# Performance work log

Measured on AMD Instinct MI355X. Metric: run time of the kernel, lower is better.

The kernel has to match this reference:

```python
import jax, jax.numpy as jnp
import numpy as np

HEADS = 8
D_MODEL = 512
D_K = D_MODEL // HEADS


def setup_inputs() -> dict:
    key = jax.random.key(0)
    ks = jax.random.split(key, 12)
    B, S = 2, 4096
    scale = 1.0 / np.sqrt(D_MODEL)
    inp = {
        "q": jax.random.normal(ks[0], (B, S, D_MODEL), jnp.float32),
        "k": jax.random.normal(ks[1], (B, S, D_MODEL), jnp.float32),
        "v": jax.random.normal(ks[2], (B, S, D_MODEL), jnp.float32),
        "mask": jax.random.randint(ks[3], (B, 1, 1, S), 0, 2, jnp.int32),
        "wq": jax.random.normal(ks[4], (D_MODEL, D_MODEL), jnp.float32) * scale,
        "bq": jnp.zeros((D_MODEL,), jnp.float32),
        "wk": jax.random.normal(ks[5], (D_MODEL, D_MODEL), jnp.float32) * scale,
        "bk": jnp.zeros((D_MODEL,), jnp.float32),
        "wv": jax.random.normal(ks[6], (D_MODEL, D_MODEL), jnp.float32) * scale,
        "bv": jnp.zeros((D_MODEL,), jnp.float32),
        "wo": jax.random.normal(ks[7], (D_MODEL, D_MODEL), jnp.float32) * scale,
        "bo": jnp.zeros((D_MODEL,), jnp.float32),
    }
    return inp


def reference(q, k, v, mask, wq, bq, wk, bk, wv, bv, wo, bo):
    B, S, _ = q.shape
    # torch nn.Linear: y = x @ W.T + b
    qh = (q @ wq.T + bq).reshape(B, S, HEADS, D_K).transpose(0, 2, 1, 3)  # b h s d
    kh = (k @ wk.T + bk).reshape(B, S, HEADS, D_K).transpose(0, 2, 1, 3)
    vh = (v @ wv.T + bv).reshape(B, S, HEADS, D_K).transpose(0, 2, 1, 3)
    scores = jnp.einsum("bhqd,bhkd->bhqk", qh, kh) / jnp.sqrt(jnp.float32(D_K))
    scores = jnp.where(mask == 0, jnp.float32(-1e9), scores)
    attn = jax.nn.softmax(scores, axis=-1)  # dropout is identity in eval mode
    out = jnp.einsum("bhqk,bhkd->bhqd", attn, vh)
    out = out.transpose(0, 2, 1, 3).reshape(B, S, D_MODEL)
    return out @ wo.T + bo
```

## Files before the change

### kernel.cpp

```cpp
#include <hip/hip_runtime.h>
#include <hip/hip_bf16.h>

#define S 4096
#define DM 512
#define HH 8
#define DK 64
#define MT 8192

typedef __attribute__((ext_vector_type(8)))  short bf16x8;
typedef __attribute__((ext_vector_type(4)))  float f32x4;
typedef __attribute__((ext_vector_type(16))) float f32x16;
typedef __attribute__((ext_vector_type(4)))  unsigned int u32x4;

#define CQ 0.18033688011112042f

__device__ __forceinline__ short f2bs(float x) {
    __hip_bfloat16 h = __float2bfloat16(x);
    return *reinterpret_cast<short*>(&h);
}

__device__ __forceinline__ bf16x8 pack8(const float4& a, const float4& b) {
    bf16x8 r;
    r[0] = f2bs(a.x); r[1] = f2bs(a.y); r[2] = f2bs(a.z); r[3] = f2bs(a.w);
    r[4] = f2bs(b.x); r[5] = f2bs(b.y); r[6] = f2bs(b.z); r[7] = f2bs(b.w);
    return r;
}

__device__ __forceinline__ unsigned cvtpk(float lo, float hi) {
    unsigned r;
    asm("v_cvt_pk_bf16_f32 %0, %1, %2" : "=v"(r) : "v"(lo), "v"(hi));
    return r;
}

__device__ __forceinline__ bf16x8 mk_pb(unsigned a, unsigned b, unsigned c, unsigned d) {
    u32x4 t; t[0] = a; t[1] = b; t[2] = c; t[3] = d;
    return __builtin_bit_cast(bf16x8, t);
}

__global__ __launch_bounds__(256, 4)
void qkv_gemm(const float* __restrict__ Xq, const float* __restrict__ Xk,
              const float* __restrict__ Xv,
              const float* __restrict__ Wq, const float* __restrict__ Wk,
              const float* __restrict__ Wv,
              const float* __restrict__ Bq, const float* __restrict__ Bk,
              const float* __restrict__ Bv,
              const int* __restrict__ mask, float* __restrict__ maskf,
              unsigned short* __restrict__ Yq, unsigned short* __restrict__ Yk,
              unsigned short* __restrict__ Yv)
{
    __shared__ char As[128 * 128];
    __shared__ char Bs[64 * 128];
    const int bid  = blockIdx.x;
    const int t = threadIdx.x;
    if (bid < 32) {
        int i = bid * 256 + t;
        maskf[i] = mask[i] ? 0.f : -3e38f;
    }
    const int work = (bid & 7) * 192 + (bid >> 3);
    const int gp   = work >> 3;
    const int mat  = gp >> 6;
    const int m0   = (gp & 63) * 128;
    const int n0   = (work & 7) * 64;
    const float* X    = mat == 0 ? Xq : (mat == 1 ? Xk : Xv);
    const float* W    = mat == 0 ? Wq : (mat == 1 ? Wk : Wv);
    const float* bias = mat == 0 ? Bq : (mat == 1 ? Bk : Bv);

    const int l = t & 63, w = t >> 6;
    const int wr = w >> 1, wc = w & 1;
    const int lr = l & 15, lg = l >> 4;
    const int srow = t >> 3, schk = t & 7;
    const int sswz = (schk ^ (srow & 7)) * 16;

    float4 fA[4][2]; float4 fB[2][2];
    auto loadA = [&](int k0) {
        #pragma unroll
        for (int i = 0; i < 4; ++i) {
            const float* p = X + (size_t)(m0 + srow + 32 * i) * DM + k0 + schk * 8;
            fA[i][0] = *(const float4*)p;
            fA[i][1] = *(const float4*)(p + 4);
        }
    };
    auto loadB = [&](int k0) {
        #pragma unroll
        for (int i = 0; i < 2; ++i) {
            const float* p = W + (size_t)(n0 + srow + 32 * i) * DM + k0 + schk * 8;
            fB[i][0] = *(const float4*)p;
            fB[i][1] = *(const float4*)(p + 4);
        }
    };

    loadA(0); loadB(0);

    f32x4 acc[4][2];
    #pragma unroll
    for (int fm = 0; fm < 4; ++fm)
        #pragma unroll
        for (int fn = 0; fn < 2; ++fn) acc[fm][fn] = f32x4{0.f, 0.f, 0.f, 0.f};

    #pragma unroll
    for (int kt = 0; kt < 8; ++kt) {
        bf16x8 wA[4], wB[2];
        #pragma unroll
        for (int i = 0; i < 4; ++i) wA[i] = pack8(fA[i][0], fA[i][1]);
        #pragma unroll
        for (int i = 0; i < 2; ++i) wB[i] = pack8(fB[i][0], fB[i][1]);

        if (kt < 7) { loadA((kt + 1) * 64); loadB((kt + 1) * 64); }

        __syncthreads();
        #pragma unroll
        for (int i = 0; i < 4; ++i)
            *(bf16x8*)(As + (srow + 32 * i) * 128 + sswz) = wA[i];
        #pragma unroll
        for (int i = 0; i < 2; ++i)
            *(bf16x8*)(Bs + (srow + 32 * i) * 128 + sswz) = wB[i];
        __syncthreads();

        #pragma unroll
        for (int kc = 0; kc < 2; ++kc) {
            bf16x8 af[4], bfr[2];
            #pragma unroll
            for (int fm = 0; fm < 4; ++fm) {
                int row = wr * 64 + fm * 16 + lr;
                af[fm] = *(const bf16x8*)(As + row * 128 + (((kc * 4 + lg) ^ (row & 7)) * 16));
            }
            #pragma unroll
            for (int fn = 0; fn < 2; ++fn) {
                int row = wc * 32 + fn * 16 + lr;
                bfr[fn] = *(const bf16x8*)(Bs + row * 128 + (((kc * 4 + lg) ^ (row & 7)) * 16));
            }
            #pragma unroll
            for (int fm = 0; fm < 4; ++fm)
                #pragma unroll
                for (int fn = 0; fn < 2; ++fn)
                    acc[fm][fn] = __builtin_amdgcn_mfma_f32_16x16x32_bf16(af[fm], bfr[fn], acc[fm][fn], 0, 0, 0);
        }
    }

    #pragma unroll
    for (int fm = 0; fm < 4; ++fm) {
        #pragma unroll
        for (int fn = 0; fn < 2; ++fn) {
            int n = n0 + wc * 32 + fn * 16 + lr;
            float bn = bias[n];
            int mbase = m0 + wr * 64 + fm * 16 + lg * 4;
            int h = n >> 6, d = n & 63;
            int bb = mbase >> 12, s0 = mbase & (S - 1);
            if (mat == 0) {
                #pragma unroll
                for (int r = 0; r < 4; ++r)
                    Yq[(((size_t)(bb * HH + h)) * S + s0 + r) * DK + d] =
                        (unsigned short)f2bs((acc[fm][fn][r] + bn) * CQ);
            } else if (mat == 1) {
                int c   = (d >> 4) & 3;
                int hi2 = (d >> 3) & 1;
                int ii  = d & 7;
                size_t blkb = ((((size_t)(bb * HH + h)) * 128 + (s0 >> 5)) * 4 + c) * 512;
                int lanebase = (s0 & 31) + 32 * hi2;
                #pragma unroll
                for (int r = 0; r < 4; ++r)
                    Yk[blkb + (size_t)(lanebase + r) * 8 + ii] =
                        (unsigned short)f2bs(acc[fm][fn][r] + bn);
            } else {
                int dt2  = (d >> 5) & 1;
                int hi_s = (s0 >> 3) & 1;
                int lane = (d & 31) + 32 * hi_s;
                size_t base = ((((size_t)(bb * HH + h)) * 256 + (s0 >> 4)) * 2 + dt2) * 512
                            + (size_t)lane * 8 + (s0 & 7);
                ushort4 u;
                u.x = (unsigned short)f2bs(acc[fm][fn][0] + bn);
                u.y = (unsigned short)f2bs(acc[fm][fn][1] + bn);
                u.z = (unsigned short)f2bs(acc[fm][fn][2] + bn);
                u.w = (unsigned short)f2bs(acc[fm][fn][3] + bn);
                *(ushort4*)(Yv + base) = u;
            }
        }
    }
}

__global__ __launch_bounds__(256, 2)
void out_gemm(const short* __restrict__ Xb, const float* __restrict__ W,
              const float* __restrict__ bias, float* __restrict__ Y)
{
    __shared__ char As[128 * 128];
    __shared__ char Bs[64 * 128];
    const int bid  = blockIdx.x;
    const int work = (bid & 7) * 64 + (bid >> 3);
    const int n0 = (work & 7) * 64;
    const int m0 = (work >> 3) * 128;

    const int t = threadIdx.x, l = t & 63, w = t >> 6;
    const int wr = w >> 1, wc = w & 1;
    const int lr = l & 15, lg = l >> 4;
    const int srow = t >> 3, schk = t & 7;
    const int sswz = (schk ^ (srow & 7)) * 16;

    float4 fB[2][2]; bf16x8 rA[4];
    auto loadA = [&](int k0) {
        #pragma unroll
        for (int i = 0; i < 4; ++i)
            rA[i] = *(const bf16x8*)(Xb + (size_t)(m0 + srow + 32 * i) * DM + k0 + schk * 8);
    };
    auto loadB = [&](int k0) {
        #pragma unroll
        for (int i = 0; i < 2; ++i) {
            const float* p = W + (size_t)(n0 + srow + 32 * i) * DM + k0 + schk * 8;
            fB[i][0] = *(const float4*)p;
            fB[i][1] = *(const float4*)(p + 4);
        }
    };

    loadA(0); loadB(0);

    f32x4 acc[4][2];
    #pragma unroll
    for (int fm = 0; fm < 4; ++fm)
        #pragma unroll
        for (int fn = 0; fn < 2; ++fn) acc[fm][fn] = f32x4{0.f, 0.f, 0.f, 0.f};

    #pragma unroll
    for (int kt = 0; kt < 8; ++kt) {
        bf16x8 wA[4], wB[2];
        #pragma unroll
        for (int i = 0; i < 4; ++i) wA[i] = rA[i];
        #pragma unroll
        for (int i = 0; i < 2; ++i) wB[i] = pack8(fB[i][0], fB[i][1]);

        if (kt < 7) { loadA((kt + 1) * 64); loadB((kt + 1) * 64); }

        __syncthreads();
        #pragma unroll
        for (int i = 0; i < 4; ++i)
            *(bf16x8*)(As + (srow + 32 * i) * 128 + sswz) = wA[i];
        #pragma unroll
        for (int i = 0; i < 2; ++i)
            *(bf16x8*)(Bs + (srow + 32 * i) * 128 + sswz) = wB[i];
        __syncthreads();

        #pragma unroll
        for (int kc = 0; kc < 2; ++kc) {
            bf16x8 af[4], bfr[2];
            #pragma unroll
            for (int fm = 0; fm < 4; ++fm) {
                int row = wr * 64 + fm * 16 + lr;
                af[fm] = *(const bf16x8*)(As + row * 128 + (((kc * 4 + lg) ^ (row & 7)) * 16));
            }
            #pragma unroll
            for (int fn = 0; fn < 2; ++fn) {
                int row = wc * 32 + fn * 16 + lr;
                bfr[fn] = *(const bf16x8*)(Bs + row * 128 + (((kc * 4 + lg) ^ (row & 7)) * 16));
            }
            #pragma unroll
            for (int fm = 0; fm < 4; ++fm)
                #pragma unroll
                for (int fn = 0; fn < 2; ++fn)
                    acc[fm][fn] = __builtin_amdgcn_mfma_f32_16x16x32_bf16(af[fm], bfr[fn], acc[fm][fn], 0, 0, 0);
        }
    }

    #pragma unroll
    for (int fm = 0; fm < 4; ++fm) {
        #pragma unroll
        for (int fn = 0; fn < 2; ++fn) {
            int n = n0 + wc * 32 + fn * 16 + lr;
            float bn = bias[n];
            int mbase = m0 + wr * 64 + fm * 16 + lg * 4;
            #pragma unroll
            for (int r = 0; r < 4; ++r)
                Y[(size_t)(mbase + r) * DM + n] = acc[fm][fn][r] + bn;
        }
    }
}

__global__ __launch_bounds__(256, 4)
void flash_mfma(const short* __restrict__ qh,
                const short* __restrict__ kfb,
                const short* __restrict__ vfb,
                const float* __restrict__ maskf,
                unsigned short* __restrict__ att)
{
    const int bid  = blockIdx.x;
    const int work = (bid & 7) * 128 + (bid >> 3);
    const int bh = work >> 6, b = bh >> 3, h = bh & 7;
    const int q0 = (work & 63) * 64;
    const int t = threadIdx.x, w = t >> 6, l = t & 63;
    const int l31 = l & 31, hi = l >> 5;
    const int kw = w & 1, qw = w >> 1;

    __shared__ float scr[2 * 64 * 33];

    const short* qg = qh + ((size_t)bh * S + q0 + qw * 32 + l31) * DK;
    bf16x8 qf[4];
    #pragma unroll
    for (int c = 0; c < 4; ++c)
        qf[c] = *(const bf16x8*)(qg + c * 16 + hi * 8);

    f32x16 oc[2];
    #pragma unroll
    for (int dt = 0; dt < 2; ++dt)
        #pragma unroll
        for (int r = 0; r < 16; ++r) oc[dt][r] = 0.f;
    float ls = 0.f;

    const short* kfp = kfb + (((size_t)bh * 128 + kw) * 4) * 512 + l * 8;
    const short* vfp = vfb + (((size_t)bh * 256 + kw * 2) * 2) * 512 + l * 8;
    const float* mp  = maskf + b * S + kw * 32 + hi * 4;

    bf16x8 kf0 = *(const bf16x8*)(kfp);
    bf16x8 kf1 = *(const bf16x8*)(kfp + 512);
    bf16x8 kf2 = *(const bf16x8*)(kfp + 1024);
    bf16x8 kf3 = *(const bf16x8*)(kfp + 1536);
    kfp += 4096;

    for (int step = 0; step < S / 64; ++step) {
        f32x4 m40 = *(const f32x4*)(mp);
        f32x4 m41 = *(const f32x4*)(mp + 8);
        f32x4 m42 = *(const f32x4*)(mp + 16);
        f32x4 m43 = *(const f32x4*)(mp + 24);
        mp += 64;
        f32x16 sc;
        #pragma unroll
        for (int o = 0; o < 4; ++o) {
            sc[o] = m40[o]; sc[4 + o] = m41[o];
            sc[8 + o] = m42[o]; sc[12 + o] = m43[o];
        }
        __builtin_amdgcn_s_setprio(1);
        sc = __builtin_amdgcn_mfma_f32_32x32x16_bf16(kf0, qf[0], sc, 0, 0, 0);
        sc = __builtin_amdgcn_mfma_f32_32x32x16_bf16(kf1, qf[1], sc, 0, 0, 0);
        sc = __builtin_amdgcn_mfma_f32_32x32x16_bf16(kf2, qf[2], sc, 0, 0, 0);
        sc = __builtin_amdgcn_mfma_f32_32x32x16_bf16(kf3, qf[3], sc, 0, 0, 0);
        __builtin_amdgcn_s_setprio(0);

        bf16x8 vf00 = *(const bf16x8*)(vfp);
        bf16x8 vf01 = *(const bf16x8*)(vfp + 512);
        bf16x8 vf10 = *(const bf16x8*)(vfp + 1024);
        bf16x8 vf11 = *(const bf16x8*)(vfp + 1536);
        vfp += 4096;

        if (step < S / 64 - 1) {
            kf0 = *(const bf16x8*)(kfp);
            kf1 = *(const bf16x8*)(kfp + 512);
            kf2 = *(const bf16x8*)(kfp + 1024);
            kf3 = *(const bf16x8*)(kfp + 1536);
            kfp += 4096;
        }

        float p[16];
        #pragma unroll
        for (int r = 0; r < 16; ++r) p[r] = exp2f(sc[r]);
        float a0 = 0.f;
        #pragma unroll
        for (int r = 0; r < 16; r += 4)
            a0 += (p[r] + p[r + 1]) + (p[r + 2] + p[r + 3]);
        ls += a0;

        unsigned A0 = cvtpk(p[0],  p[1]),  B0 = cvtpk(p[2],  p[3]);
        unsigned A1 = cvtpk(p[4],  p[5]),  B1 = cvtpk(p[6],  p[7]);
        unsigned A2 = cvtpk(p[8],  p[9]),  B2 = cvtpk(p[10], p[11]);
        unsigned A3 = cvtpk(p[12], p[13]), B3 = cvtpk(p[14], p[15]);
        asm("v_permlane32_swap_b32 %0, %1" : "+v"(A0), "+v"(A1));
        asm("v_permlane32_swap_b32 %0, %1" : "+v"(B0), "+v"(B1));
        asm("v_permlane32_swap_b32 %0, %1" : "+v"(A2), "+v"(A3));
        asm("v_permlane32_swap_b32 %0, %1" : "+v"(B2), "+v"(B3));
        bf16x8 pb0 = mk_pb(A0, B0, A1, B1);
        bf16x8 pb1 = mk_pb(A2, B2, A3, B3);

        __builtin_amdgcn_s_setprio(1);
        oc[0] = __builtin_amdgcn_mfma_f32_32x32x16_bf16(vf00, pb0, oc[0], 0, 0, 0);
        oc[1] = __builtin_amdgcn_mfma_f32_32x32x16_bf16(vf01, pb0, oc[1], 0, 0, 0);
        oc[0] = __builtin_amdgcn_mfma_f32_32x32x16_bf16(vf10, pb1, oc[0], 0, 0, 0);
        oc[1] = __builtin_amdgcn_mfma_f32_32x32x16_bf16(vf11, pb1, oc[1], 0, 0, 0);
        __builtin_amdgcn_s_setprio(0);
    }

    __syncthreads();
    float* pp = scr + (size_t)(qw * 64 + l) * 33;
    if (kw == 1) {
        #pragma unroll
        for (int r = 0; r < 16; ++r) { pp[r] = oc[0][r]; pp[16 + r] = oc[1][r]; }
        pp[32] = ls;
    }
    __syncthreads();
    if (kw == 0) {
        #pragma unroll
        for (int r = 0; r < 16; ++r) { oc[0][r] += pp[r]; oc[1][r] += pp[16 + r]; }
        ls += pp[32];
        ls += __shfl_xor(ls, 32);
        const float linv = 1.0f / ls;
        unsigned short* ap = att + ((size_t)(b * S + q0 + qw * 32 + l31)) * DM + h * DK;
        #pragma unroll
        for (int dt = 0; dt < 2; ++dt)
            #pragma unroll
            for (int g = 0; g < 4; ++g) {
                uint2 u;
                u.x = cvtpk(oc[dt][g * 4 + 0] * linv, oc[dt][g * 4 + 1] * linv);
                u.y = cvtpk(oc[dt][g * 4 + 2] * linv, oc[dt][g * 4 + 3] * linv);
                *(uint2*)(ap + dt * 32 + g * 8 + hi * 4) = u;
            }
    }
}

extern "C" void kernel_launch(void* const* d_in, const int* in_sizes, int n_in,
                              void* d_out, int out_size, void* d_ws, size_t ws_size,
                              hipStream_t stream) {
    const float* q    = (const float*)d_in[0];
    const float* k    = (const float*)d_in[1];
    const float* v    = (const float*)d_in[2];
    const int*   mask = (const int*)  d_in[3];
    const float* wq   = (const float*)d_in[4];
    const float* bq   = (const float*)d_in[5];
    const float* wk   = (const float*)d_in[6];
    const float* bk   = (const float*)d_in[7];
    const float* wv   = (const float*)d_in[8];
    const float* bv   = (const float*)d_in[9];
    const float* wo   = (const float*)d_in[10];
    const float* bo   = (const float*)d_in[11];
    float* out = (float*)d_out;

    char* wsb = (char*)d_ws;
    unsigned short* qh    = (unsigned short*)(wsb);
    unsigned short* kfb   = (unsigned short*)(wsb + (size_t)8  * 1024 * 1024);
    unsigned short* vfb   = (unsigned short*)(wsb + (size_t)16 * 1024 * 1024);
    unsigned short* att   = (unsigned short*)(wsb + (size_t)24 * 1024 * 1024);
    float*          maskf = (float*)         (wsb + (size_t)32 * 1024 * 1024);

    dim3 blk(256);
    qkv_gemm<<<dim3(1536), blk, 0, stream>>>(q, k, v, wq, wk, wv, bq, bk, bv,
                                     mask, maskf, qh, kfb, vfb);

    flash_mfma<<<dim3(1024), blk, 0, stream>>>((const short*)qh, (const short*)kfb,
                                     (const short*)vfb, maskf, att);

    out_gemm<<<dim3(512), blk, 0, stream>>>((const short*)att, wo, bo, out);
}
```

Before: 165.5 us.

## Stage K/V tiles and mask into LDS with double-buffered async global loads

Replaces the per-wave direct global loads of K, V fragments and mask values in the flash attention loop with cooperative global_load_lds copies into two LDS buffers. Each step stages the next tile while computing on the current one, and block-wide barriers separate the phases. This is meant to remove redundant global traffic, since both query-wave pairs share the same K/V, and to hide memory latency. In exchange it adds two __syncthreads per pair of steps and 33KB of LDS, which may reduce occupancy.

```diff
diff --git a/kernel.cpp b/kernel.cpp
--- a/kernel.cpp
+++ b/kernel.cpp
@@ -35,6 +35,17 @@
 __device__ __forceinline__ bf16x8 mk_pb(unsigned a, unsigned b, unsigned c, unsigned d) {
     u32x4 t; t[0] = a; t[1] = b; t[2] = c; t[3] = d;
     return __builtin_bit_cast(bf16x8, t);
+}
+
+__device__ __forceinline__ void gld_lds16(const void* gp, void* lp) {
+    __builtin_amdgcn_global_load_lds(
+        (const __attribute__((address_space(1))) void*)gp,
+        (__attribute__((address_space(3))) void*)lp, 16, 0, 0);
+}
+__device__ __forceinline__ void gld_lds4(const void* gp, void* lp) {
+    __builtin_amdgcn_global_load_lds(
+        (const __attribute__((address_space(1))) void*)gp,
+        (__attribute__((address_space(3))) void*)lp, 4, 0, 0);
 }
 
 __global__ __launch_bounds__(256, 4)
@@ -287,7 +298,11 @@
     const int l31 = l & 31, hi = l >> 5;
     const int kw = w & 1, qw = w >> 1;
 
-    __shared__ float scr[2 * 64 * 33];
+    __shared__ char sBuf[2 * 16384 + 2 * 256];
+    char*  B0 = sBuf;
+    char*  B1 = sBuf + 16384;
+    float* M0 = (float*)(sBuf + 32768);
+    float* M1 = (float*)(sBuf + 32768 + 256);
 
     const short* qg = qh + ((size_t)bh * S + q0 + qw * 32 + l31) * DK;
     bf16x8 qf[4];
@@ -302,28 +317,39 @@
         for (int r = 0; r < 16; ++r) oc[dt][r] = 0.f;
     float ls = 0.f;
 
-    const short* kfp = kfb + (((size_t)bh * 128 + kw) * 4) * 512 + l * 8;
-    const short* vfp = vfb + (((size_t)bh * 256 + kw * 2) * 2) * 512 + l * 8;
-    const float* mp  = maskf + b * S + kw * 32 + hi * 4;
-
-    bf16x8 kf0 = *(const bf16x8*)(kfp);
-    bf16x8 kf1 = *(const bf16x8*)(kfp + 512);
-    bf16x8 kf2 = *(const bf16x8*)(kfp + 1024);
-    bf16x8 kf3 = *(const bf16x8*)(kfp + 1536);
-    kfp += 4096;
-
-    for (int step = 0; step < S / 64; ++step) {
-        f32x4 m40 = *(const f32x4*)(mp);
-        f32x4 m41 = *(const f32x4*)(mp + 8);
-        f32x4 m42 = *(const f32x4*)(mp + 16);
-        f32x4 m43 = *(const f32x4*)(mp + 24);
-        mp += 64;
+    const char* kg0 = (const char*)(kfb + (size_t)bh * 262144) + (size_t)l * 16;
+    const char* vg0 = (const char*)(vfb + (size_t)bh * 262144) + (size_t)l * 16;
+    const char* mg0 = (const char*)(maskf + b * S) + (size_t)l * 4;
+
+    auto stage = [&](char* dst, float* mdst, int step) {
+        const char* kg = kg0 + (size_t)step * 8192;
+        const char* vg = vg0 + (size_t)step * 8192;
+        #pragma unroll
+        for (int i = 0; i < 4; ++i) {
+            int chunk = w * 4 + i;
+            const char* g = (chunk < 8) ? (kg + chunk * 1024) : (vg + (chunk - 8) * 1024);
+            gld_lds16(g, dst + chunk * 1024);
+        }
+        if (w == 0) gld_lds4(mg0 + (size_t)step * 256, mdst);
+    };
+
+    auto compute = [&](const char* kv, const float* mlds) {
+        const char* mb = (const char*)mlds + kw * 128 + hi * 16;
+        f32x4 m40 = *(const f32x4*)(mb);
+        f32x4 m41 = *(const f32x4*)(mb + 32);
+        f32x4 m42 = *(const f32x4*)(mb + 64);
+        f32x4 m43 = *(const f32x4*)(mb + 96);
         f32x16 sc;
         #pragma unroll
         for (int o = 0; o < 4; ++o) {
             sc[o] = m40[o]; sc[4 + o] = m41[o];
             sc[8 + o] = m42[o]; sc[12 + o] = m43[o];
         }
+        const char* kbase = kv + kw * 4096 + l * 16;
+        bf16x8 kf0 = *(const bf16x8*)(kbase);
+        bf16x8 kf1 = *(const bf16x8*)(kbase + 1024);
+        bf16x8 kf2 = *(const bf16x8*)(kbase + 2048);
+        bf16x8 kf3 = *(const bf16x8*)(kbase + 3072);
         __builtin_amdgcn_s_setprio(1);
         sc = __builtin_amdgcn_mfma_f32_32x32x16_bf16(kf0, qf[0], sc, 0, 0, 0);
         sc = __builtin_amdgcn_mfma_f32_32x32x16_bf16(kf1, qf[1], sc, 0, 0, 0);
@@ -331,19 +357,11 @@
         sc = __builtin_amdgcn_mfma_f32_32x32x16_bf16(kf3, qf[3], sc, 0, 0, 0);
         __builtin_amdgcn_s_setprio(0);
 
-        bf16x8 vf00 = *(const bf16x8*)(vfp);
-        bf16x8 vf01 = *(const bf16x8*)(vfp + 512);
-        bf16x8 vf10 = *(const bf16x8*)(vfp + 1024);
-        bf16x8 vf11 = *(const bf16x8*)(vfp + 1536);
-        vfp += 4096;
-
-        if (step < S / 64 - 1) {
-            kf0 = *(const bf16x8*)(kfp);
-            kf1 = *(const bf16x8*)(kfp + 512);
-            kf2 = *(const bf16x8*)(kfp + 1024);
-            kf3 = *(const bf16x8*)(kfp + 1536);
-            kfp += 4096;
-        }
+        const char* vbase = kv + 8192 + kw * 4096 + l * 16;
+        bf16x8 vf00 = *(const bf16x8*)(vbase);
+        bf16x8 vf01 = *(const bf16x8*)(vbase + 1024);
+        bf16x8 vf10 = *(const bf16x8*)(vbase + 2048);
+        bf16x8 vf11 = *(const bf16x8*)(vbase + 3072);
 
         float p[16];
         #pragma unroll
@@ -354,16 +372,16 @@
             a0 += (p[r] + p[r + 1]) + (p[r + 2] + p[r + 3]);
         ls += a0;
 
-        unsigned A0 = cvtpk(p[0],  p[1]),  B0 = cvtpk(p[2],  p[3]);
-        unsigned A1 = cvtpk(p[4],  p[5]),  B1 = cvtpk(p[6],  p[7]);
-        unsigned A2 = cvtpk(p[8],  p[9]),  B2 = cvtpk(p[10], p[11]);
-        unsigned A3 = cvtpk(p[12], p[13]), B3 = cvtpk(p[14], p[15]);
+        unsigned A0 = cvtpk(p[0],  p[1]),  B0r = cvtpk(p[2],  p[3]);
+        unsigned A1 = cvtpk(p[4],  p[5]),  B1r = cvtpk(p[6],  p[7]);
+        unsigned A2 = cvtpk(p[8],  p[9]),  B2r = cvtpk(p[10], p[11]);
+        unsigned A3 = cvtpk(p[12], p[13]), B3r = cvtpk(p[14], p[15]);
         asm("v_permlane32_swap_b32 %0, %1" : "+v"(A0), "+v"(A1));
-        asm("v_permlane32_swap_b32 %0, %1" : "+v"(B0), "+v"(B1));
+        asm("v_permlane32_swap_b32 %0, %1" : "+v"(B0r), "+v"(B1r));
         asm("v_permlane32_swap_b32 %0, %1" : "+v"(A2), "+v"(A3));
-        asm("v_permlane32_swap_b32 %0, %1" : "+v"(B2), "+v"(B3));
-        bf16x8 pb0 = mk_pb(A0, B0, A1, B1);
-        bf16x8 pb1 = mk_pb(A2, B2, A3, B3);
+        asm("v_permlane32_swap_b32 %0, %1" : "+v"(B2r), "+v"(B3r));
+        bf16x8 pb0 = mk_pb(A0, B0r, A1, B1r);
+        bf16x8 pb1 = mk_pb(A2, B2r, A3, B3r);
 
         __builtin_amdgcn_s_setprio(1);
         oc[0] = __builtin_amdgcn_mfma_f32_32x32x16_bf16(vf00, pb0, oc[0], 0, 0, 0);
@@ -371,10 +389,24 @@
         oc[0] = __builtin_amdgcn_mfma_f32_32x32x16_bf16(vf10, pb1, oc[0], 0, 0, 0);
         oc[1] = __builtin_amdgcn_mfma_f32_32x32x16_bf16(vf11, pb1, oc[1], 0, 0, 0);
         __builtin_amdgcn_s_setprio(0);
-    }
-
+    };
+
+    stage(B0, M0, 0);
     __syncthreads();
-    float* pp = scr + (size_t)(qw * 64 + l) * 33;
+
+    const int NT = S / 64;
+    for (int it = 0; it < NT / 2; ++it) {
+        const int s0 = it * 2;
+        stage(B1, M1, s0 + 1);
+        compute(B0, M0);
+        __syncthreads();
+        if (s0 + 2 < NT) stage(B0, M0, s0 + 2);
+        compute(B1, M1);
+        __syncthreads();
+    }
+
+    float* scr = (float*)sBuf;
+    float* pp  = scr + (size_t)(qw * 64 + l) * 33;
     if (kw == 1) {
         #pragma unroll
         for (int r = 0; r < 16; ++r) { pp[r] = oc[0][r]; pp[16 + r] = oc[1][r]; }
```

Measured after the change: 162.2 us (median of 3 runs). -2.0%, faster.
